# Kernel tuning notes

Hardware: AMD Instinct MI355X
Metric: run time of the kernel (lower is better)

The kernel has to match this reference:

```python
import jax, jax.numpy as jnp
import numpy as np

EPS = 1e-8  # torch CosineSimilarity eps


def _cosine_sim_matrix(x, y):
    # x: [Nx, D], y: [Ny, D] -> [Nx, Ny] cosine similarity via normalized GEMM
    xn = x / jnp.maximum(jnp.linalg.norm(x, axis=-1, keepdims=True), EPS)
    yn = y / jnp.maximum(jnp.linalg.norm(y, axis=-1, keepdims=True), EPS)
    return xn @ yn.T


def setup_inputs() -> dict:
    key = jax.random.key(0)
    k1, k2, k3, k4 = jax.random.split(key, 4)
    N, D, C = 4096, 512, 100
    inst_embed = jax.random.normal(k1, (N, D), dtype=jnp.float32)
    proxy = jax.random.normal(k2, (N, D), dtype=jnp.float32)
    # binary positive-selection mask per class over the batch
    negative_mask = (jax.random.uniform(k3, (C, N)) > 0.5).astype(jnp.float32)
    labels = jax.random.randint(k4, (N,), 0, C, dtype=jnp.int64)
    temperature = jnp.float32(0.1)
    margin = jnp.float32(0.0)
    return {"inst_embed": inst_embed, "proxy": proxy,
            "negative_mask": negative_mask, "labels": labels,
            "temperature": temperature, "margin": margin}


def reference(inst_embed, proxy, negative_mask, labels, temperature, margin):
    # [N, N] similarity matrices
    p2i = _cosine_sim_matrix(proxy, inst_embed)
    i2i = _cosine_sim_matrix(inst_embed, inst_embed)
    p2i_zone = jnp.exp((p2i - margin) / temperature)
    i2i_zone = jnp.exp((i2i - margin) / temperature)
    mask = negative_mask[labels]  # [N, N]
    p2i_num = (p2i_zone * mask).sum(axis=1)
    i2i_num = (i2i_zone * mask).sum(axis=1)
    p2i_den = p2i_zone.sum(axis=1)
    i2i_den = i2i_zone.sum(axis=1)
    p2i_loss = -jnp.log(temperature * (p2i_num / p2i_den)).mean()
    i2i_loss = -jnp.log(temperature * (i2i_num / i2i_den)).mean()
    return p2i_loss + i2i_loss
```

## Files before the change

kernel.cpp:

```cpp
#include <hip/hip_runtime.h>
#include <hip/hip_bf16.h>

#define D_DIM 512
#define KSTEPS 16
#define BM 128
#define BN 32
#define GRIDY 8

typedef __bf16 bf16x8 __attribute__((ext_vector_type(8)));
typedef float  f32x4  __attribute__((ext_vector_type(4)));

__device__ __forceinline__ unsigned short f2bf_rne(float x) {
    unsigned int u = __float_as_uint(x);
    u += 0x7FFFu + ((u >> 16) & 1u);
    return (unsigned short)(u >> 16);
}

__device__ __forceinline__ void g2l16(const void* g, void* l) {
    __builtin_amdgcn_global_load_lds(
        (const __attribute__((address_space(1))) unsigned int*)g,
        (__attribute__((address_space(3))) unsigned int*)l, 16, 0, 0);
}

__global__ __launch_bounds__(256) void normalize_rows(
    const float* __restrict__ inst, const float* __restrict__ proxy,
    unsigned short* __restrict__ instb, unsigned short* __restrict__ proxyb,
    float* __restrict__ nd, int N)
{
    const int lane = threadIdx.x & 63;
    const int wave = threadIdx.x >> 6;
    const int base = blockIdx.x * 16 + wave * 4;
    #pragma unroll
    for (int i = 0; i < 4; ++i) {
        const int row = base + i;
        const float* src;
        unsigned short* dst;
        if (row < N) { src = inst  + (size_t)row * D_DIM;        dst = instb  + (size_t)row * D_DIM; }
        else         { src = proxy + (size_t)(row - N) * D_DIM;  dst = proxyb + (size_t)(row - N) * D_DIM; }
        float4 v0 = ((const float4*)src)[lane * 2];
        float4 v1 = ((const float4*)src)[lane * 2 + 1];
        float ss = v0.x*v0.x + v0.y*v0.y + v0.z*v0.z + v0.w*v0.w
                 + v1.x*v1.x + v1.y*v1.y + v1.z*v1.z + v1.w*v1.w;
        #pragma unroll
        for (int off = 32; off > 0; off >>= 1) ss += __shfl_xor(ss, off, 64);
        const float inv = 1.0f / fmaxf(sqrtf(ss), 1e-8f);
        ushort4 o0, o1;
        o0.x = f2bf_rne(v0.x * inv); o0.y = f2bf_rne(v0.y * inv);
        o0.z = f2bf_rne(v0.z * inv); o0.w = f2bf_rne(v0.w * inv);
        o1.x = f2bf_rne(v1.x * inv); o1.y = f2bf_rne(v1.y * inv);
        o1.z = f2bf_rne(v1.z * inv); o1.w = f2bf_rne(v1.w * inv);
        ((ushort4*)dst)[lane * 2]     = o0;
        ((ushort4*)dst)[lane * 2 + 1] = o1;
    }
    if (blockIdx.x < 16)
        ((float4*)nd)[blockIdx.x * 256 + threadIdx.x] = make_float4(0.f, 0.f, 0.f, 0.f);
}

__global__ __launch_bounds__(256, 1) void fused_scores(
    const unsigned short* __restrict__ instb,
    const unsigned short* __restrict__ proxyb,
    const float* __restrict__ negmask,
    const int*  __restrict__ labels,
    const float* __restrict__ temp_p,
    const float* __restrict__ margin_p,
    float* __restrict__ nd,
    int N, int colsPerBlock)
{
    __shared__ unsigned short Bt0[BN * D_DIM];
    __shared__ unsigned short Bt1[BN * D_DIM];

    const int tid  = threadIdx.x;
    const int lane = tid & 63;
    const int wave = tid >> 6;
    const int quad = lane >> 4;
    const int l16  = lane & 15;

    const int row0 = blockIdx.x * BM + wave * 32;

    const float temp  = *temp_p;
    const float scale = 1.44269504088896340736f / temp;
    const float bias  = -(*margin_p) * scale;

    bf16x8 Ap0[KSTEPS], Ai0[KSTEPS], Ap1[KSTEPS], Ai1[KSTEPS];
    {
        const unsigned short* p0 = proxyb + (size_t)(row0 + l16)      * D_DIM + quad * 8;
        const unsigned short* i0 = instb  + (size_t)(row0 + l16)      * D_DIM + quad * 8;
        const unsigned short* p1 = proxyb + (size_t)(row0 + 16 + l16) * D_DIM + quad * 8;
        const unsigned short* i1 = instb  + (size_t)(row0 + 16 + l16) * D_DIM + quad * 8;
        #pragma unroll
        for (int ks = 0; ks < KSTEPS; ks++) {
            Ap0[ks] = *(const bf16x8*)(p0 + ks * 32);
            Ai0[ks] = *(const bf16x8*)(i0 + ks * 32);
            Ap1[ks] = *(const bf16x8*)(p1 + ks * 32);
            Ai1[ks] = *(const bf16x8*)(i1 + ks * 32);
        }
    }

    int lab[2][4];
    #pragma unroll
    for (int g = 0; g < 2; g++)
        #pragma unroll
        for (int r = 0; r < 4; r++)
            lab[g][r] = labels[row0 + g * 16 + quad * 4 + r];

    float numP[2][4] = {}, denP[2][4] = {};
    float numI[2][4] = {}, denI[2][4] = {};

    const int j0base = blockIdx.y * colsPerBlock;
    const int nt     = colsPerBlock / BN;

    auto stage = [&](unsigned short (&B)[BN * D_DIM], int t) {
        const int j0 = j0base + t * BN;
        #pragma unroll
        for (int it = 0; it < BN / 4; ++it) {
            const int br = it * 4 + wave;
            const unsigned short* src =
                instb + (size_t)(j0 + br) * D_DIM + ((lane ^ (br & 7)) * 8);
            g2l16(src, &B[br * D_DIM]);
        }
    };

    auto compute = [&](unsigned short (&B)[BN * D_DIM], int t) {
        const int j0 = j0base + t * BN;
        float mk[2][2][4];
        #pragma unroll
        for (int g = 0; g < 2; ++g)
            #pragma unroll
            for (int c = 0; c < 2; ++c)
                #pragma unroll
                for (int r = 0; r < 4; ++r)
                    mk[g][c][r] = negmask[(size_t)lab[g][r] * N + (j0 + c * 16 + l16)];

        f32x4 aP0[2] = {}, aI0[2] = {}, aP1[2] = {}, aI1[2] = {};
        #pragma unroll
        for (int ks = 0; ks < KSTEPS; ++ks) {
            #pragma unroll
            for (int cg = 0; cg < 2; ++cg) {
                const int rB  = cg * 16 + l16;
                const int chs = (ks * 4 + quad) ^ (rB & 7);
                bf16x8 b = *(const bf16x8*)&B[(size_t)rB * D_DIM + chs * 8];
                aP0[cg] = __builtin_amdgcn_mfma_f32_16x16x32_bf16(Ap0[ks], b, aP0[cg], 0, 0, 0);
                aI0[cg] = __builtin_amdgcn_mfma_f32_16x16x32_bf16(Ai0[ks], b, aI0[cg], 0, 0, 0);
                aP1[cg] = __builtin_amdgcn_mfma_f32_16x16x32_bf16(Ap1[ks], b, aP1[cg], 0, 0, 0);
                aI1[cg] = __builtin_amdgcn_mfma_f32_16x16x32_bf16(Ai1[ks], b, aI1[cg], 0, 0, 0);
            }
        }

        #pragma unroll
        for (int cg = 0; cg < 2; ++cg) {
            #pragma unroll
            for (int r = 0; r < 4; ++r) {
                float zp0 = exp2f(aP0[cg][r] * scale + bias);
                float zi0 = exp2f(aI0[cg][r] * scale + bias);
                float zp1 = exp2f(aP1[cg][r] * scale + bias);
                float zi1 = exp2f(aI1[cg][r] * scale + bias);
                denP[0][r] += zp0; numP[0][r] += zp0 * mk[0][cg][r];
                denI[0][r] += zi0; numI[0][r] += zi0 * mk[0][cg][r];
                denP[1][r] += zp1; numP[1][r] += zp1 * mk[1][cg][r];
                denI[1][r] += zi1; numI[1][r] += zi1 * mk[1][cg][r];
            }
        }
    };

    stage(Bt0, 0);
    __syncthreads();
    for (int t = 0; t < nt; t += 2) {
        stage(Bt1, t + 1);
        compute(Bt0, t);
        __syncthreads();
        if (t + 2 < nt) stage(Bt0, t + 2);
        compute(Bt1, t + 1);
        __syncthreads();
    }

    #pragma unroll
    for (int g = 0; g < 2; ++g) {
        #pragma unroll
        for (int r = 0; r < 4; ++r) {
            float np = numP[g][r], dp = denP[g][r], ni = numI[g][r], di = denI[g][r];
            #pragma unroll
            for (int off = 8; off > 0; off >>= 1) {
                np += __shfl_down(np, off, 16);
                dp += __shfl_down(dp, off, 16);
                ni += __shfl_down(ni, off, 16);
                di += __shfl_down(di, off, 16);
            }
            if (l16 == 0) {
                const int row = row0 + g * 16 + quad * 4 + r;
                atomicAdd(&nd[row],         np);
                atomicAdd(&nd[N + row],     dp);
                atomicAdd(&nd[2 * N + row], ni);
                atomicAdd(&nd[3 * N + row], di);
            }
        }
    }
}

__global__ __launch_bounds__(1024) void loss_reduce(
    const float* __restrict__ nd, const float* __restrict__ temp_p,
    float* __restrict__ out, int N)
{
    const float t = *temp_p;
    float s = 0.f;
    for (int i = threadIdx.x; i < N; i += 1024) {
        s += (logf(nd[N + i])     - logf(nd[i]));
        s += (logf(nd[3 * N + i]) - logf(nd[2 * N + i]));
    }
    #pragma unroll
    for (int off = 32; off > 0; off >>= 1) s += __shfl_down(s, off, 64);
    __shared__ float wss[16];
    if ((threadIdx.x & 63) == 0) wss[threadIdx.x >> 6] = s;
    __syncthreads();
    if (threadIdx.x < 16) {
        float v = wss[threadIdx.x];
        #pragma unroll
        for (int off = 8; off > 0; off >>= 1) v += __shfl_down(v, off, 16);
        if (threadIdx.x == 0) out[0] = v / (float)N - 2.0f * logf(t);
    }
}

extern "C" void kernel_launch(void* const* d_in, const int* in_sizes, int n_in,
                              void* d_out, int out_size, void* d_ws, size_t ws_size,
                              hipStream_t stream)
{
    const float* inst     = (const float*)d_in[0];
    const float* proxy    = (const float*)d_in[1];
    const float* negmask  = (const float*)d_in[2];
    const int*   labels   = (const int*)d_in[3];
    const float* temp_p   = (const float*)d_in[4];
    const float* margin_p = (const float*)d_in[5];
    float* out = (float*)d_out;

    const int N = in_sizes[3];

    unsigned short* instb  = (unsigned short*)d_ws;
    unsigned short* proxyb = instb + (size_t)N * D_DIM;
    float* nd = (float*)(proxyb + (size_t)N * D_DIM);

    normalize_rows<<<2 * N / 16, 256, 0, stream>>>(inst, proxy, instb, proxyb, nd, N);
    dim3 grid(N / BM, GRIDY);
    fused_scores<<<grid, 256, 0, stream>>>(instb, proxyb, negmask, labels,
                                           temp_p, margin_p, nd, N, N / GRIDY);
    loss_reduce<<<1, 1024, 0, stream>>>(nd, temp_p, out, N);
}
```

Baseline: 129.5 us.

## Single-buffer LDS, raise occupancy, split columns finer, fuse final reduction via last-block

Replaces the double-buffered B tile with a single LDS buffer and sets launch bounds to two blocks per CU, so two workgroups can overlap instead of pipelining within one. GRIDY goes from 8 to 16, which doubles the number of blocks and shortens each block's column range. The loss_reduce kernel is removed: the last block to finish, found with an atomic counter, computes the final log-sum, which saves one launch. MFMA sections are wrapped in s_setprio. The costs are a lost in-block load/compute overlap, register pressure to fit two blocks, and twice as many atomics on nd.

```diff
diff --git a/kernel.cpp b/kernel.cpp
--- a/kernel.cpp
+++ b/kernel.cpp
@@ -5,7 +5,7 @@
 #define KSTEPS 16
 #define BM 128
 #define BN 32
-#define GRIDY 8
+#define GRIDY 16
 
 typedef __bf16 bf16x8 __attribute__((ext_vector_type(8)));
 typedef float  f32x4  __attribute__((ext_vector_type(4)));
@@ -25,7 +25,7 @@
 __global__ __launch_bounds__(256) void normalize_rows(
     const float* __restrict__ inst, const float* __restrict__ proxy,
     unsigned short* __restrict__ instb, unsigned short* __restrict__ proxyb,
-    float* __restrict__ nd, int N)
+    float* __restrict__ nd, int* __restrict__ ctr, int N)
 {
     const int lane = threadIdx.x & 63;
     const int wave = threadIdx.x >> 6;
@@ -54,9 +54,10 @@
     }
     if (blockIdx.x < 16)
         ((float4*)nd)[blockIdx.x * 256 + threadIdx.x] = make_float4(0.f, 0.f, 0.f, 0.f);
-}
-
-__global__ __launch_bounds__(256, 1) void fused_scores(
+    if (blockIdx.x == 16 && threadIdx.x == 0) *ctr = 0;
+}
+
+__global__ __launch_bounds__(256, 2) void fused_scores(
     const unsigned short* __restrict__ instb,
     const unsigned short* __restrict__ proxyb,
     const float* __restrict__ negmask,
@@ -64,10 +65,11 @@
     const float* __restrict__ temp_p,
     const float* __restrict__ margin_p,
     float* __restrict__ nd,
+    int* __restrict__ ctr,
+    float* __restrict__ out,
     int N, int colsPerBlock)
 {
-    __shared__ unsigned short Bt0[BN * D_DIM];
-    __shared__ unsigned short Bt1[BN * D_DIM];
+    __shared__ unsigned short Bt[BN * D_DIM];
 
     const int tid  = threadIdx.x;
     const int lane = tid & 63;
@@ -75,7 +77,11 @@
     const int quad = lane >> 4;
     const int l16  = lane & 15;
 
-    const int row0 = blockIdx.x * BM + wave * 32;
+    const int bx = blockIdx.x >> 4;
+    const int by = blockIdx.x & 15;
+
+    const int row0   = bx * BM + wave * 32;
+    const int j0base = by * colsPerBlock;
 
     const float temp  = *temp_p;
     const float scale = 1.44269504088896340736f / temp;
@@ -106,22 +112,18 @@
     float numP[2][4] = {}, denP[2][4] = {};
     float numI[2][4] = {}, denI[2][4] = {};
 
-    const int j0base = blockIdx.y * colsPerBlock;
-    const int nt     = colsPerBlock / BN;
-
-    auto stage = [&](unsigned short (&B)[BN * D_DIM], int t) {
-        const int j0 = j0base + t * BN;
-        #pragma unroll
-        for (int it = 0; it < BN / 4; ++it) {
+    for (int jt = 0; jt < colsPerBlock; jt += BN) {
+        const int j0 = j0base + jt;
+        __syncthreads();
+        #pragma unroll
+        for (int it = 0; it < BN / 4; it++) {
             const int br = it * 4 + wave;
             const unsigned short* src =
                 instb + (size_t)(j0 + br) * D_DIM + ((lane ^ (br & 7)) * 8);
-            g2l16(src, &B[br * D_DIM]);
-        }
-    };
-
-    auto compute = [&](unsigned short (&B)[BN * D_DIM], int t) {
-        const int j0 = j0base + t * BN;
+            g2l16(src, &Bt[(size_t)br * D_DIM]);
+        }
+        __syncthreads();
+
         float mk[2][2][4];
         #pragma unroll
         for (int g = 0; g < 2; ++g)
@@ -132,19 +134,21 @@
                     mk[g][c][r] = negmask[(size_t)lab[g][r] * N + (j0 + c * 16 + l16)];
 
         f32x4 aP0[2] = {}, aI0[2] = {}, aP1[2] = {}, aI1[2] = {};
+        __builtin_amdgcn_s_setprio(1);
         #pragma unroll
         for (int ks = 0; ks < KSTEPS; ++ks) {
             #pragma unroll
             for (int cg = 0; cg < 2; ++cg) {
                 const int rB  = cg * 16 + l16;
                 const int chs = (ks * 4 + quad) ^ (rB & 7);
-                bf16x8 b = *(const bf16x8*)&B[(size_t)rB * D_DIM + chs * 8];
+                bf16x8 b = *(const bf16x8*)&Bt[(size_t)rB * D_DIM + chs * 8];
                 aP0[cg] = __builtin_amdgcn_mfma_f32_16x16x32_bf16(Ap0[ks], b, aP0[cg], 0, 0, 0);
                 aI0[cg] = __builtin_amdgcn_mfma_f32_16x16x32_bf16(Ai0[ks], b, aI0[cg], 0, 0, 0);
                 aP1[cg] = __builtin_amdgcn_mfma_f32_16x16x32_bf16(Ap1[ks], b, aP1[cg], 0, 0, 0);
                 aI1[cg] = __builtin_amdgcn_mfma_f32_16x16x32_bf16(Ai1[ks], b, aI1[cg], 0, 0, 0);
             }
         }
+        __builtin_amdgcn_s_setprio(0);
 
         #pragma unroll
         for (int cg = 0; cg < 2; ++cg) {
@@ -160,17 +164,6 @@
                 denI[1][r] += zi1; numI[1][r] += zi1 * mk[1][cg][r];
             }
         }
-    };
-
-    stage(Bt0, 0);
-    __syncthreads();
-    for (int t = 0; t < nt; t += 2) {
-        stage(Bt1, t + 1);
-        compute(Bt0, t);
-        __syncthreads();
-        if (t + 2 < nt) stage(Bt0, t + 2);
-        compute(Bt1, t + 1);
-        __syncthreads();
     }
 
     #pragma unroll
@@ -194,28 +187,33 @@
             }
         }
     }
-}
-
-__global__ __launch_bounds__(1024) void loss_reduce(
-    const float* __restrict__ nd, const float* __restrict__ temp_p,
-    float* __restrict__ out, int N)
-{
-    const float t = *temp_p;
-    float s = 0.f;
-    for (int i = threadIdx.x; i < N; i += 1024) {
-        s += (logf(nd[N + i])     - logf(nd[i]));
-        s += (logf(nd[3 * N + i]) - logf(nd[2 * N + i]));
-    }
-    #pragma unroll
-    for (int off = 32; off > 0; off >>= 1) s += __shfl_down(s, off, 64);
-    __shared__ float wss[16];
-    if ((threadIdx.x & 63) == 0) wss[threadIdx.x >> 6] = s;
+
+    __shared__ int isLast;
+    __threadfence();
+    if (tid == 0) {
+        int prev = __hip_atomic_fetch_add(ctr, 1, __ATOMIC_ACQ_REL,
+                                          __HIP_MEMORY_SCOPE_AGENT);
+        isLast = (prev == (int)gridDim.x - 1);
+    }
     __syncthreads();
-    if (threadIdx.x < 16) {
-        float v = wss[threadIdx.x];
-        #pragma unroll
-        for (int off = 8; off > 0; off >>= 1) v += __shfl_down(v, off, 16);
-        if (threadIdx.x == 0) out[0] = v / (float)N - 2.0f * logf(t);
+    if (isLast) {
+        float s = 0.f;
+        for (int i = tid; i < N; i += 256) {
+            float pn = __hip_atomic_load(&nd[i],         __ATOMIC_RELAXED, __HIP_MEMORY_SCOPE_AGENT);
+            float pd = __hip_atomic_load(&nd[N + i],     __ATOMIC_RELAXED, __HIP_MEMORY_SCOPE_AGENT);
+            float in_ = __hip_atomic_load(&nd[2 * N + i], __ATOMIC_RELAXED, __HIP_MEMORY_SCOPE_AGENT);
+            float id = __hip_atomic_load(&nd[3 * N + i], __ATOMIC_RELAXED, __HIP_MEMORY_SCOPE_AGENT);
+            s += (logf(pd) - logf(pn)) + (logf(id) - logf(in_));
+        }
+        #pragma unroll
+        for (int off = 32; off > 0; off >>= 1) s += __shfl_down(s, off, 64);
+        float* wss = (float*)Bt;
+        __syncthreads();
+        if ((tid & 63) == 0) wss[tid >> 6] = s;
+        __syncthreads();
+        if (tid == 0)
+            out[0] = (wss[0] + wss[1] + wss[2] + wss[3]) / (float)N
+                   - 2.0f * logf(temp);
     }
 }
 
@@ -236,10 +234,11 @@
     unsigned short* instb  = (unsigned short*)d_ws;
     unsigned short* proxyb = instb + (size_t)N * D_DIM;
     float* nd = (float*)(proxyb + (size_t)N * D_DIM);
-
-    normalize_rows<<<2 * N / 16, 256, 0, stream>>>(inst, proxy, instb, proxyb, nd, N);
-    dim3 grid(N / BM, GRIDY);
-    fused_scores<<<grid, 256, 0, stream>>>(instb, proxyb, negmask, labels,
-                                           temp_p, margin_p, nd, N, N / GRIDY);
-    loss_reduce<<<1, 1024, 0, stream>>>(nd, temp_p, out, N);
-}
+    int*  ctr = (int*)(nd + 4 * (size_t)N);
+
+    normalize_rows<<<2 * N / 16, 256, 0, stream>>>(inst, proxy, instb, proxyb,
+                                                   nd, ctr, N);
+    fused_scores<<<(N / BM) * GRIDY, 256, 0, stream>>>(instb, proxyb, negmask,
+                                                       labels, temp_p, margin_p,
+                                                       nd, ctr, out, N, N / GRIDY);
+}
```

Result: slower. 271.6 us (+109.7%).
